# Performance work log

Hardware: AMD Instinct MI355X
Metric: run time of the kernel (lower is better)

## Reference

```python
import jax, jax.numpy as jnp
import numpy as np

MASK_OUT_VALUE = -10000.0


def setup_inputs() -> dict:
    key = jax.random.key(0)
    k1, k2, k3 = jax.random.split(key, 3)
    B, H, S, D = 2, 16, 2048, 64
    query = jax.random.normal(k1, (B, H, S, D), dtype=jnp.float32)
    key_t = jax.random.normal(k2, (B, H, S, D), dtype=jnp.float32)
    value = jax.random.normal(k3, (B, H, S, D), dtype=jnp.float32)
    # causal mask: (1, 1, S, S), True where attention is allowed
    mask = jnp.tril(jnp.ones((S, S), dtype=bool))[None, None, :, :]
    return {"query": query, "key": key_t, "value": value, "mask": mask}


def reference(query, key, value, mask):
    # scores: (B, H, S, S)
    scale = 1.0 / jnp.sqrt(jnp.asarray(query.shape[-1], query.dtype))
    attn_scores = jnp.einsum("bhqd,bhkd->bhqk", query, key) * scale
    attn_scores = jnp.where(mask, attn_scores,
                            jnp.asarray(MASK_OUT_VALUE, attn_scores.dtype))
    attn_weights = jax.nn.softmax(attn_scores, axis=-1)
    # dropout is identity (p=0 / eval mode)
    attn_output = jnp.einsum("bhqk,bhkd->bhqd", attn_weights, value)
    return attn_output
```

## Files before the change

### kernel.cpp

```cpp
#include <hip/hip_runtime.h>
#include <math.h>


#define S_LEN   2048
#define D_HEAD  64
#define SCALE_L2E 0.18033688011112042f
#define FIXM    8.0f

using bf16x8 = __attribute__((ext_vector_type(8))) short;
using f32x4  = __attribute__((ext_vector_type(4))) float;
using uint4v = __attribute__((ext_vector_type(4))) unsigned int;

__device__ __forceinline__ unsigned int rnd_bf(float f) {
  return __float_as_uint(f) + 0x8000u;
}
__device__ __forceinline__ unsigned short f2bf(float f) {
  return (unsigned short)(rnd_bf(f) >> 16);
}

__device__ __forceinline__ void gl_lds16(const unsigned short* g, unsigned short* l) {
  __builtin_amdgcn_global_load_lds(
      (const __attribute__((address_space(1))) unsigned int*)g,
      (__attribute__((address_space(3))) unsigned int*)l, 16, 0, 0);
}

__device__ __forceinline__ unsigned int cvtpk_bf16(float lo, float hi) {
  unsigned int r;
  asm("v_cvt_pk_bf16_f32 %0, %1, %2" : "=v"(r) : "v"(lo), "v"(hi));
  return r;
}
__device__ __forceinline__ void swap32(unsigned int& a, unsigned int& b) {
  asm("v_permlane32_swap_b32 %0, %1" : "+v"(a), "+v"(b));
}
__device__ __forceinline__ void swap16(unsigned int& a, unsigned int& b) {
  asm("v_permlane16_swap_b32 %0, %1" : "+v"(a), "+v"(b));
}

template <int CTRL>
__device__ __forceinline__ float dppf(float x) {
  return __builtin_bit_cast(float,
      __builtin_amdgcn_update_dpp(0, __builtin_bit_cast(int, x), CTRL, 0xF, 0xF, false));
}
__device__ __forceinline__ float rowsum16(float x) {
  x += dppf<0xB1>(x);
  x += dppf<0x4E>(x);
  x += dppf<0x124>(x);
  x += dppf<0x128>(x);
  return x;
}

__global__ __launch_bounds__(256, 4)
void prep(const float* __restrict__ Kg, const float* __restrict__ Vg,
          unsigned short* __restrict__ Kb, unsigned short* __restrict__ Vt)
{
  __shared__ __align__(16) unsigned short Lt[64][72];
  const int j = blockIdx.x, t = threadIdx.x;
  const int bh = j >> 4, seg = j & 15;
  const size_t base = (size_t)bh * (S_LEN * D_HEAD) + (size_t)seg * 128 * D_HEAD;
#pragma unroll
  for (int i = 0; i < 8; ++i) {
    const size_t idx = base + i * 1024 + t * 4;
    const f32x4 v = *(const f32x4*)(Kg + idx);
    uint2 pk;
    pk.x = (rnd_bf(v[1]) & 0xFFFF0000u) | (rnd_bf(v[0]) >> 16);
    pk.y = (rnd_bf(v[3]) & 0xFFFF0000u) | (rnd_bf(v[2]) >> 16);
    *(uint2*)(Kb + idx) = pk;
  }
  for (int h = 0; h < 2; ++h) {
    const int s0 = seg * 128 + h * 64;
    __syncthreads();
#pragma unroll
    for (int pp = 0; pp < 4; ++pp) {
      const int r = t >> 2;
      const int d0 = (t & 3) * 4 + pp * 16;
      const f32x4 v = *(const f32x4*)(Vg + (size_t)bh * (S_LEN * D_HEAD)
                                         + (size_t)(s0 + r) * D_HEAD + d0);
#pragma unroll
      for (int e = 0; e < 4; ++e) Lt[d0 + e][r] = f2bf(v[e]);
    }
    __syncthreads();
#pragma unroll
    for (int q = 0; q < 2; ++q) {
      const int d = t >> 2, ch = (t & 3) + 4 * q;
      *(uint4*)(Vt + (size_t)(bh * 64 + d) * S_LEN + s0 + ch * 8) =
          *(const uint4*)&Lt[d][ch * 8];
    }
  }
}

__global__ __launch_bounds__(256, 2)
void fa(const float* __restrict__ Qg, const unsigned short* __restrict__ Kb,
        const unsigned short* __restrict__ Vt, float* __restrict__ Og)
{
  __shared__ unsigned short Ks[2][2][64][64];
  __shared__ unsigned short Vs[2][2][64][64];

  const int id = blockIdx.x;
  const int bh = id & 31;
  const int pr = id >> 5;

  const int t    = threadIdx.x;
  const int w    = t >> 6;
  const int lane = t & 63;
  const int c    = lane & 15;
  const int quad = lane >> 4;

  const float* __restrict__ Qb = Qg + (size_t)bh * (S_LEN * D_HEAD);
  float* __restrict__ Ob = Og + (size_t)bh * (S_LEN * D_HEAD);

  const int tr0 = pr, tr1 = 31 - pr;

  int fOff[4][2];
#pragma unroll
  for (int ci = 0; ci < 4; ++ci)
#pragma unroll
    for (int h = 0; h < 2; ++h)
      fOff[ci][h] = ((ci * 16 + c) << 6) + (((h * 4 + quad) ^ (c & 7)) << 3);

  bf16x8 ones;
#pragma unroll
  for (int j = 0; j < 8; ++j) ones[j] = (short)0x3F80;

  const int rl = lane >> 3;
  const int jj = (lane & 7) ^ rl;
  auto stage1 = [&](int kt, int buf, int sub) {
#pragma unroll
    for (int n = 0; n < 2; ++n) {
      const int row = w * 16 + n * 8 + rl;
      gl_lds16(Kb + (((size_t)(bh * S_LEN + kt * 64 + row)) << 6) + jj * 8,
               &Ks[buf][sub][w * 16 + n * 8][0]);
      gl_lds16(Vt + (((size_t)(bh * 64 + row)) << 11) + kt * 64 + jj * 8,
               &Vs[buf][sub][w * 16 + n * 8][0]);
    }
  };
  auto stage_pair = [&](int it, int tr, int buf) {
    const int k0 = 2 * it;
    stage1(k0, buf, 0);
    if (k0 + 1 <= tr) stage1(k0 + 1, buf, 1);
  };

  auto smpack = [&](f32x4* sc, bf16x8& p0, bf16x8& p1) {
    unsigned int Wt[4][2];
#pragma unroll
    for (int ci = 0; ci < 4; ++ci) {
#pragma unroll
      for (int r = 0; r < 4; ++r)
        sc[ci][r] = __builtin_amdgcn_exp2f(sc[ci][r]);
      Wt[ci][0] = cvtpk_bf16(sc[ci][0], sc[ci][1]);
      Wt[ci][1] = cvtpk_bf16(sc[ci][2], sc[ci][3]);
    }
    unsigned int a00 = Wt[0][0], a02 = Wt[1][0]; swap32(a00, a02); swap16(a00, a02);
    unsigned int a01 = Wt[0][1], a03 = Wt[1][1]; swap32(a01, a03); swap16(a01, a03);
    unsigned int a10 = Wt[2][0], a12 = Wt[3][0]; swap32(a10, a12); swap16(a10, a12);
    unsigned int a11 = Wt[2][1], a13 = Wt[3][1]; swap32(a11, a13); swap16(a11, a13);
    p0 = __builtin_bit_cast(bf16x8, (uint4v){a00, a01, a02, a03});
    p1 = __builtin_bit_cast(bf16x8, (uint4v){a10, a11, a12, a13});
  };

  bf16x8 qa[2];
  f32x4 oa[4];
  f32x4 lacc;

  int buf = 0;
  stage_pair(0, tr0, 0);

#pragma unroll 1
  for (int ph = 0; ph < 2; ++ph) {
    const int tr    = ph ? tr1 : tr0;
    const int row0  = tr * 64 + w * 16;
    const int iters = (tr + 2) >> 1;

    {
      const float* qp = Qb + (size_t)(row0 + c) * D_HEAD + quad * 8;
#pragma unroll
      for (int h = 0; h < 2; ++h) {
        f32x4 a0 = *(const f32x4*)(qp + 32 * h);
        f32x4 a1 = *(const f32x4*)(qp + 32 * h + 4);
#pragma unroll
        for (int j = 0; j < 4; ++j) {
          qa[h][j]     = (short)f2bf(a0[j] * SCALE_L2E);
          qa[h][4 + j] = (short)f2bf(a1[j] * SCALE_L2E);
        }
      }
    }
#pragma unroll
    for (int i = 0; i < 4; ++i) oa[i] = (f32x4){0.f, 0.f, 0.f, 0.f};
    lacc = (f32x4){0.f, 0.f, 0.f, 0.f};

#pragma unroll 1
    for (int it = 0; it < iters; ++it) {
      __syncthreads();
      if (it + 1 < iters)  stage_pair(it + 1, tr, buf ^ 1);
      else if (ph == 0)    stage_pair(0, tr1, buf ^ 1);

      const int kt0 = 2 * it, kt1 = kt0 + 1;
      const bool has1 = (kt1 <= tr);

      const unsigned short* ks0 = &Ks[buf][0][0][0];
      const unsigned short* ks1 = &Ks[buf][1][0][0];
      bf16x8 kf0[4][2], kf1[4][2];
#pragma unroll
      for (int ci = 0; ci < 4; ++ci)
#pragma unroll
        for (int h = 0; h < 2; ++h)
          kf0[ci][h] = *(const bf16x8*)(ks0 + fOff[ci][h]);
      if (has1)
#pragma unroll
        for (int ci = 0; ci < 4; ++ci)
#pragma unroll
          for (int h = 0; h < 2; ++h)
            kf1[ci][h] = *(const bf16x8*)(ks1 + fOff[ci][h]);

      __builtin_amdgcn_s_setprio(1);
      f32x4 sc0[4], sc1[4];
#pragma unroll
      for (int ci = 0; ci < 4; ++ci) {
        f32x4 acc = (f32x4){-FIXM, -FIXM, -FIXM, -FIXM};
        acc = __builtin_amdgcn_mfma_f32_16x16x32_bf16(kf0[ci][0], qa[0], acc, 0, 0, 0);
        acc = __builtin_amdgcn_mfma_f32_16x16x32_bf16(kf0[ci][1], qa[1], acc, 0, 0, 0);
        sc0[ci] = acc;
      }
      if (has1)
#pragma unroll
        for (int ci = 0; ci < 4; ++ci) {
          f32x4 acc = (f32x4){-FIXM, -FIXM, -FIXM, -FIXM};
          acc = __builtin_amdgcn_mfma_f32_16x16x32_bf16(kf1[ci][0], qa[0], acc, 0, 0, 0);
          acc = __builtin_amdgcn_mfma_f32_16x16x32_bf16(kf1[ci][1], qa[1], acc, 0, 0, 0);
          sc1[ci] = acc;
        }

      const unsigned short* vs0 = &Vs[buf][0][0][0];
      const unsigned short* vs1 = &Vs[buf][1][0][0];
      bf16x8 vf0[4][2], vf1[4][2];
#pragma unroll
      for (int ci = 0; ci < 4; ++ci)
#pragma unroll
        for (int h = 0; h < 2; ++h)
          vf0[ci][h] = *(const bf16x8*)(vs0 + fOff[ci][h]);
      if (has1)
#pragma unroll
        for (int ci = 0; ci < 4; ++ci)
#pragma unroll
          for (int h = 0; h < 2; ++h)
            vf1[ci][h] = *(const bf16x8*)(vs1 + fOff[ci][h]);

      if (kt0 == tr) {
        const int grow = row0 + c;
#pragma unroll
        for (int ci = 0; ci < 4; ++ci)
#pragma unroll
          for (int r = 0; r < 4; ++r)
            if (kt0 * 64 + ci * 16 + quad * 4 + r > grow) sc0[ci][r] = -1e30f;
      }
      if (has1 && kt1 == tr) {
        const int grow = row0 + c;
#pragma unroll
        for (int ci = 0; ci < 4; ++ci)
#pragma unroll
          for (int r = 0; r < 4; ++r)
            if (kt1 * 64 + ci * 16 + quad * 4 + r > grow) sc1[ci][r] = -1e30f;
      }

      bf16x8 paA0, paA1, paB0, paB1;
      smpack(sc0, paA0, paA1);
      if (has1) smpack(sc1, paB0, paB1);

#pragma unroll
      for (int ci = 0; ci < 4; ++ci) {
        oa[ci] = __builtin_amdgcn_mfma_f32_16x16x32_bf16(paA0, vf0[ci][0], oa[ci], 0, 0, 0);
        oa[ci] = __builtin_amdgcn_mfma_f32_16x16x32_bf16(paA1, vf0[ci][1], oa[ci], 0, 0, 0);
      }
      lacc = __builtin_amdgcn_mfma_f32_16x16x32_bf16(paA0, ones, lacc, 0, 0, 0);
      lacc = __builtin_amdgcn_mfma_f32_16x16x32_bf16(paA1, ones, lacc, 0, 0, 0);
      if (has1) {
#pragma unroll
        for (int ci = 0; ci < 4; ++ci) {
          oa[ci] = __builtin_amdgcn_mfma_f32_16x16x32_bf16(paB0, vf1[ci][0], oa[ci], 0, 0, 0);
          oa[ci] = __builtin_amdgcn_mfma_f32_16x16x32_bf16(paB1, vf1[ci][1], oa[ci], 0, 0, 0);
        }
        lacc = __builtin_amdgcn_mfma_f32_16x16x32_bf16(paB0, ones, lacc, 0, 0, 0);
        lacc = __builtin_amdgcn_mfma_f32_16x16x32_bf16(paB1, ones, lacc, 0, 0, 0);
      }
      __builtin_amdgcn_s_setprio(0);

      buf ^= 1;
    }

    {
      float inv[4];
#pragma unroll
      for (int r = 0; r < 4; ++r) inv[r] = 1.0f / lacc[r];
#pragma unroll
      for (int ci = 0; ci < 4; ++ci)
#pragma unroll
        for (int r = 0; r < 4; ++r)
          Ob[(size_t)(row0 + quad * 4 + r) * D_HEAD + ci * 16 + c] =
              oa[ci][r] * inv[r];
    }
  }
}

__global__ __launch_bounds__(256, 4)
void fa_fb(const float* __restrict__ Qg, const float* __restrict__ Kg,
           const float* __restrict__ Vg, float* __restrict__ Og)
{
  __shared__ __align__(16) unsigned short Ksh[64][72];
  __shared__ __align__(16) unsigned short Vsh[64][72];
  __shared__ __align__(16) unsigned short Psh[4][16][72];
  const int id = blockIdx.x;
  const int bh = id & 31;
  const int p  = id >> 5;
  const int t    = threadIdx.x;
  const int w    = t >> 6;
  const int lane = t & 63;
  const int c    = lane & 15;
  const int quad = lane >> 4;
  const size_t base = (size_t)bh * (S_LEN * D_HEAD);
  const float* __restrict__ Qb = Qg + base;
  const float* __restrict__ Kb = Kg + base;
  const float* __restrict__ Vb = Vg + base;
  float* __restrict__ Ob = Og + base;
  const int wv   = w & 1;
  const int row0 = (w >= 2) ? (S_LEN - 32 * (p + 1) + 16 * wv) : (32 * p + 16 * wv);
  const int ktdiag = row0 >> 6;
  const int ktmax  = (S_LEN - 1 - 32 * p) >> 6;
  bf16x8 qa[2];
  {
    const float* qp = Qb + (size_t)(row0 + c) * D_HEAD + quad * 8;
#pragma unroll
    for (int h = 0; h < 2; ++h) {
      f32x4 a0 = *(const f32x4*)(qp + 32 * h);
      f32x4 a1 = *(const f32x4*)(qp + 32 * h + 4);
#pragma unroll
      for (int j = 0; j < 4; ++j) {
        qa[h][j]     = (short)f2bf(a0[j] * SCALE_L2E);
        qa[h][4 + j] = (short)f2bf(a1[j] * SCALE_L2E);
      }
    }
  }
  f32x4 oa[4];
  float ls[4];
#pragma unroll
  for (int i = 0; i < 4; ++i) {
    oa[i] = (f32x4){0.f, 0.f, 0.f, 0.f};
    ls[i] = 0.f;
  }
  for (int kt = 0; kt <= ktmax; ++kt) {
    __syncthreads();
    {
      const int cp = t & 15;
      const int rg = t >> 4;
      const int col0 = cp * 4;
      const int sw = (cp >> 2) << 3;
#pragma unroll
      for (int i = 0; i < 4; ++i) {
        const int row = i * 16 + rg;
        const size_t goff = (size_t)(kt * 64 + row) * D_HEAD + col0;
        const f32x4 kv = *(const f32x4*)(Kb + goff);
        const f32x4 vv = *(const f32x4*)(Vb + goff);
        const unsigned int k01 = (rnd_bf(kv[1]) & 0xFFFF0000u) | (rnd_bf(kv[0]) >> 16);
        const unsigned int k23 = (rnd_bf(kv[3]) & 0xFFFF0000u) | (rnd_bf(kv[2]) >> 16);
        *(uint2*)&Ksh[row][col0] = make_uint2(k01, k23);
        const int kz = row ^ sw;
#pragma unroll
        for (int e = 0; e < 4; ++e)
          Vsh[col0 + e][kz] = f2bf(vv[e]);
      }
    }
    __syncthreads();
    if (kt <= ktdiag) {
      bf16x8 kf[4][2], vf[4][2];
#pragma unroll
      for (int ci = 0; ci < 4; ++ci) {
        kf[ci][0] = *(const bf16x8*)&Ksh[ci * 16 + c][quad * 8];
        kf[ci][1] = *(const bf16x8*)&Ksh[ci * 16 + c][32 + quad * 8];
        vf[ci][0] = *(const bf16x8*)&Vsh[ci * 16 + c][(quad ^ ci) * 8];
        vf[ci][1] = *(const bf16x8*)&Vsh[ci * 16 + c][32 + ((quad ^ ci) * 8)];
      }
      f32x4 sc[4];
#pragma unroll
      for (int ci = 0; ci < 4; ++ci) {
        f32x4 acc = (f32x4){-FIXM, -FIXM, -FIXM, -FIXM};
        acc = __builtin_amdgcn_mfma_f32_16x16x32_bf16(qa[0], kf[ci][0], acc, 0, 0, 0);
        acc = __builtin_amdgcn_mfma_f32_16x16x32_bf16(qa[1], kf[ci][1], acc, 0, 0, 0);
        sc[ci] = acc;
      }
      if (kt == ktdiag) {
#pragma unroll
        for (int ci = 0; ci < 4; ++ci) {
          const int gcol = kt * 64 + ci * 16 + c;
#pragma unroll
          for (int r = 0; r < 4; ++r)
            if (gcol > row0 + quad * 4 + r) sc[ci][r] = -1e30f;
        }
      }
#pragma unroll
      for (int ci = 0; ci < 4; ++ci)
#pragma unroll
        for (int r = 0; r < 4; ++r)
          sc[ci][r] = __builtin_amdgcn_exp2f(sc[ci][r]);
#pragma unroll
      for (int r = 0; r < 4; ++r)
        ls[r] += (sc[0][r] + sc[1][r]) + (sc[2][r] + sc[3][r]);
#pragma unroll
      for (int ci = 0; ci < 4; ++ci)
#pragma unroll
        for (int r = 0; r < 4; ++r) {
          const int prow = quad * 4 + r;
          Psh[w][prow][(ci * 16 + c) ^ ((prow >> 3) << 3)] = f2bf(sc[ci][r]);
        }
      const int px = (c >> 3) << 3;
      const bf16x8 pa0 = *(const bf16x8*)&Psh[w][c][(quad * 8) ^ px];
      const bf16x8 pa1 = *(const bf16x8*)&Psh[w][c][((32 + quad * 8)) ^ px];
#pragma unroll
      for (int ci = 0; ci < 4; ++ci) {
        oa[ci] = __builtin_amdgcn_mfma_f32_16x16x32_bf16(pa0, vf[ci][0], oa[ci], 0, 0, 0);
        oa[ci] = __builtin_amdgcn_mfma_f32_16x16x32_bf16(pa1, vf[ci][1], oa[ci], 0, 0, 0);
      }
    }
  }
  {
    float inv[4];
#pragma unroll
    for (int r = 0; r < 4; ++r) inv[r] = 1.0f / rowsum16(ls[r]);
#pragma unroll
    for (int ci = 0; ci < 4; ++ci)
#pragma unroll
      for (int r = 0; r < 4; ++r)
        Ob[(size_t)(row0 + quad * 4 + r) * D_HEAD + ci * 16 + c] = oa[ci][r] * inv[r];
  }
}

extern "C" void kernel_launch(void* const* d_in, const int* in_sizes, int n_in,
                              void* d_out, int out_size, void* d_ws, size_t ws_size,
                              hipStream_t stream) {
  (void)in_sizes; (void)n_in; (void)out_size;
  const float* Q = (const float*)d_in[0];
  const float* K = (const float*)d_in[1];
  const float* V = (const float*)d_in[2];
  float* O = (float*)d_out;
  const size_t NEED = 2ull * 32 * S_LEN * D_HEAD * 2;
  if (ws_size >= NEED) {
    unsigned short* Kb = (unsigned short*)d_ws;
    unsigned short* Vt = Kb + (size_t)32 * S_LEN * D_HEAD;
    prep<<<dim3(512), dim3(256), 0, stream>>>(K, V, Kb, Vt);
    fa<<<dim3(512), dim3(256), 0, stream>>>(Q, Kb, Vt, O);
  } else {
    fa_fb<<<dim3(1024), dim3(256), 0, stream>>>(Q, K, V, O);
  }
}
```

Measured before the change: 130.8 us.

## Fuse K/V bf16 conversion into attention kernel, drop prep pass

```diff
diff --git a/kernel.cpp b/kernel.cpp
--- a/kernel.cpp
+++ b/kernel.cpp
@@ -18,12 +18,6 @@
   return (unsigned short)(rnd_bf(f) >> 16);
 }
 
-__device__ __forceinline__ void gl_lds16(const unsigned short* g, unsigned short* l) {
-  __builtin_amdgcn_global_load_lds(
-      (const __attribute__((address_space(1))) unsigned int*)g,
-      (__attribute__((address_space(3))) unsigned int*)l, 16, 0, 0);
-}
-
 __device__ __forceinline__ unsigned int cvtpk_bf16(float lo, float hi) {
   unsigned int r;
   asm("v_cvt_pk_bf16_f32 %0, %1, %2" : "=v"(r) : "v"(lo), "v"(hi));
@@ -36,64 +30,12 @@
   asm("v_permlane16_swap_b32 %0, %1" : "+v"(a), "+v"(b));
 }
 
-template <int CTRL>
-__device__ __forceinline__ float dppf(float x) {
-  return __builtin_bit_cast(float,
-      __builtin_amdgcn_update_dpp(0, __builtin_bit_cast(int, x), CTRL, 0xF, 0xF, false));
-}
-__device__ __forceinline__ float rowsum16(float x) {
-  x += dppf<0xB1>(x);
-  x += dppf<0x4E>(x);
-  x += dppf<0x124>(x);
-  x += dppf<0x128>(x);
-  return x;
-}
-
-__global__ __launch_bounds__(256, 4)
-void prep(const float* __restrict__ Kg, const float* __restrict__ Vg,
-          unsigned short* __restrict__ Kb, unsigned short* __restrict__ Vt)
-{
-  __shared__ __align__(16) unsigned short Lt[64][72];
-  const int j = blockIdx.x, t = threadIdx.x;
-  const int bh = j >> 4, seg = j & 15;
-  const size_t base = (size_t)bh * (S_LEN * D_HEAD) + (size_t)seg * 128 * D_HEAD;
-#pragma unroll
-  for (int i = 0; i < 8; ++i) {
-    const size_t idx = base + i * 1024 + t * 4;
-    const f32x4 v = *(const f32x4*)(Kg + idx);
-    uint2 pk;
-    pk.x = (rnd_bf(v[1]) & 0xFFFF0000u) | (rnd_bf(v[0]) >> 16);
-    pk.y = (rnd_bf(v[3]) & 0xFFFF0000u) | (rnd_bf(v[2]) >> 16);
-    *(uint2*)(Kb + idx) = pk;
-  }
-  for (int h = 0; h < 2; ++h) {
-    const int s0 = seg * 128 + h * 64;
-    __syncthreads();
-#pragma unroll
-    for (int pp = 0; pp < 4; ++pp) {
-      const int r = t >> 2;
-      const int d0 = (t & 3) * 4 + pp * 16;
-      const f32x4 v = *(const f32x4*)(Vg + (size_t)bh * (S_LEN * D_HEAD)
-                                         + (size_t)(s0 + r) * D_HEAD + d0);
-#pragma unroll
-      for (int e = 0; e < 4; ++e) Lt[d0 + e][r] = f2bf(v[e]);
-    }
-    __syncthreads();
-#pragma unroll
-    for (int q = 0; q < 2; ++q) {
-      const int d = t >> 2, ch = (t & 3) + 4 * q;
-      *(uint4*)(Vt + (size_t)(bh * 64 + d) * S_LEN + s0 + ch * 8) =
-          *(const uint4*)&Lt[d][ch * 8];
-    }
-  }
-}
-
 __global__ __launch_bounds__(256, 2)
-void fa(const float* __restrict__ Qg, const unsigned short* __restrict__ Kb,
-        const unsigned short* __restrict__ Vt, float* __restrict__ Og)
+void fa(const float* __restrict__ Qg, const float* __restrict__ Kg,
+        const float* __restrict__ Vg, float* __restrict__ Og)
 {
   __shared__ unsigned short Ks[2][2][64][64];
-  __shared__ unsigned short Vs[2][2][64][64];
+  __shared__ unsigned short Vs[2][2][64][72];
 
   const int id = blockIdx.x;
   const int bh = id & 31;
@@ -105,8 +47,11 @@
   const int c    = lane & 15;
   const int quad = lane >> 4;
 
-  const float* __restrict__ Qb = Qg + (size_t)bh * (S_LEN * D_HEAD);
-  float* __restrict__ Ob = Og + (size_t)bh * (S_LEN * D_HEAD);
+  const size_t base = (size_t)bh * (S_LEN * D_HEAD);
+  const float* __restrict__ Qb = Qg + base;
+  const float* __restrict__ Kb = Kg + base;
+  const float* __restrict__ Vb = Vg + base;
+  float* __restrict__ Ob = Og + base;
 
   const int tr0 = pr, tr1 = 31 - pr;
 
@@ -116,27 +61,62 @@
 #pragma unroll
     for (int h = 0; h < 2; ++h)
       fOff[ci][h] = ((ci * 16 + c) << 6) + (((h * 4 + quad) ^ (c & 7)) << 3);
+  int vOff[4][2];
+#pragma unroll
+  for (int ci = 0; ci < 4; ++ci)
+#pragma unroll
+    for (int h = 0; h < 2; ++h)
+      vOff[ci][h] = (ci * 16 + c) * 72 + (((h * 4 + quad) ^ ci) << 3);
 
   bf16x8 ones;
 #pragma unroll
   for (int j = 0; j < 8; ++j) ones[j] = (short)0x3F80;
 
-  const int rl = lane >> 3;
-  const int jj = (lane & 7) ^ rl;
-  auto stage1 = [&](int kt, int buf, int sub) {
-#pragma unroll
-    for (int n = 0; n < 2; ++n) {
-      const int row = w * 16 + n * 8 + rl;
-      gl_lds16(Kb + (((size_t)(bh * S_LEN + kt * 64 + row)) << 6) + jj * 8,
-               &Ks[buf][sub][w * 16 + n * 8][0]);
-      gl_lds16(Vt + (((size_t)(bh * 64 + row)) << 11) + kt * 64 + jj * 8,
-               &Vs[buf][sub][w * 16 + n * 8][0]);
-    }
+  const int sr  = lane >> 4;
+  const int sc4 = lane & 15;
+
+  f32x4 kreg[2][4], vreg[2][4];
+  auto issue_loads = [&](int n_it, int n_tr) {
+    const int k0 = 2 * n_it;
+#pragma unroll
+    for (int sub = 0; sub < 2; ++sub)
+      if (k0 + sub <= n_tr)
+#pragma unroll
+        for (int p = 0; p < 4; ++p) {
+          const int row = (k0 + sub) * 64 + w * 16 + p * 4 + sr;
+          kreg[sub][p] = *(const f32x4*)(Kb + (size_t)row * 64 + sc4 * 4);
+          vreg[sub][p] = *(const f32x4*)(Vb + (size_t)row * 64 + sc4 * 4);
+        }
   };
-  auto stage_pair = [&](int it, int tr, int buf) {
-    const int k0 = 2 * it;
-    stage1(k0, buf, 0);
-    if (k0 + 1 <= tr) stage1(k0 + 1, buf, 1);
+  auto write_K = [&](int n_it, int n_tr, int nb) {
+    const int k0 = 2 * n_it;
+#pragma unroll
+    for (int sub = 0; sub < 2; ++sub)
+      if (k0 + sub <= n_tr)
+#pragma unroll
+        for (int p = 0; p < 4; ++p) {
+          const int rl = w * 16 + p * 4 + sr;
+          uint2 pk;
+          pk.x = cvtpk_bf16(kreg[sub][p][0], kreg[sub][p][1]);
+          pk.y = cvtpk_bf16(kreg[sub][p][2], kreg[sub][p][3]);
+          const int jl = (sc4 >> 1) ^ (rl & 7);
+          *(uint2*)&Ks[nb][sub][rl][jl * 8 + (sc4 & 1) * 4] = pk;
+        }
+  };
+  auto write_V = [&](int n_it, int n_tr, int nb) {
+    const int k0 = 2 * n_it;
+#pragma unroll
+    for (int sub = 0; sub < 2; ++sub)
+      if (k0 + sub <= n_tr)
+#pragma unroll
+        for (int p = 0; p < 4; ++p) {
+          const int sl = w * 16 + p * 4 + sr;
+#pragma unroll
+          for (int e = 0; e < 4; ++e) {
+            const int d = sc4 * 4 + e;
+            Vs[nb][sub][d][sl ^ ((d >> 4) << 3)] = f2bf(vreg[sub][p][e]);
+          }
+        }
   };
 
   auto smpack = [&](f32x4* sc, bf16x8& p0, bf16x8& p1) {
@@ -162,7 +142,9 @@
   f32x4 lacc;
 
   int buf = 0;
-  stage_pair(0, tr0, 0);
+  issue_loads(0, tr0);
+  write_K(0, tr0, 0);
+  write_V(0, tr0, 0);
 
 #pragma unroll 1
   for (int ph = 0; ph < 2; ++ph) {
@@ -190,8 +172,12 @@
 #pragma unroll 1
     for (int it = 0; it < iters; ++it) {
       __syncthreads();
-      if (it + 1 < iters)  stage_pair(it + 1, tr, buf ^ 1);
-      else if (ph == 0)    stage_pair(0, tr1, buf ^ 1);
+
+      int n_it = -1, n_tr = 0;
+      if (it + 1 < iters)      { n_it = it + 1; n_tr = tr;  }
+      else if (ph == 0)        { n_it = 0;      n_tr = tr1; }
+      const bool do_stage = (n_it >= 0);
+      if (do_stage) issue_loads(n_it, n_tr);
 
       const int kt0 = 2 * it, kt1 = kt0 + 1;
       const bool has1 = (kt1 <= tr);
@@ -229,6 +215,8 @@
           sc1[ci] = acc;
         }
 
+      if (do_stage) write_K(n_it, n_tr, buf ^ 1);
+
       const unsigned short* vs0 = &Vs[buf][0][0][0];
       const unsigned short* vs1 = &Vs[buf][1][0][0];
       bf16x8 vf0[4][2], vf1[4][2];
@@ -236,13 +224,13 @@
       for (int ci = 0; ci < 4; ++ci)
 #pragma unroll
         for (int h = 0; h < 2; ++h)
-          vf0[ci][h] = *(const bf16x8*)(vs0 + fOff[ci][h]);
+          vf0[ci][h] = *(const bf16x8*)(vs0 + vOff[ci][h]);
       if (has1)
 #pragma unroll
         for (int ci = 0; ci < 4; ++ci)
 #pragma unroll
           for (int h = 0; h < 2; ++h)
-            vf1[ci][h] = *(const bf16x8*)(vs1 + fOff[ci][h]);
+            vf1[ci][h] = *(const bf16x8*)(vs1 + vOff[ci][h]);
 
       if (kt0 == tr) {
         const int grow = row0 + c;
@@ -264,6 +252,8 @@
       bf16x8 paA0, paA1, paB0, paB1;
       smpack(sc0, paA0, paA1);
       if (has1) smpack(sc1, paB0, paB1);
+
+      if (do_stage) write_V(n_it, n_tr, buf ^ 1);
 
 #pragma unroll
       for (int ci = 0; ci < 4; ++ci) {
@@ -300,152 +290,13 @@
   }
 }
 
-__global__ __launch_bounds__(256, 4)
-void fa_fb(const float* __restrict__ Qg, const float* __restrict__ Kg,
-           const float* __restrict__ Vg, float* __restrict__ Og)
-{
-  __shared__ __align__(16) unsigned short Ksh[64][72];
-  __shared__ __align__(16) unsigned short Vsh[64][72];
-  __shared__ __align__(16) unsigned short Psh[4][16][72];
-  const int id = blockIdx.x;
-  const int bh = id & 31;
-  const int p  = id >> 5;
-  const int t    = threadIdx.x;
-  const int w    = t >> 6;
-  const int lane = t & 63;
-  const int c    = lane & 15;
-  const int quad = lane >> 4;
-  const size_t base = (size_t)bh * (S_LEN * D_HEAD);
-  const float* __restrict__ Qb = Qg + base;
-  const float* __restrict__ Kb = Kg + base;
-  const float* __restrict__ Vb = Vg + base;
-  float* __restrict__ Ob = Og + base;
-  const int wv   = w & 1;
-  const int row0 = (w >= 2) ? (S_LEN - 32 * (p + 1) + 16 * wv) : (32 * p + 16 * wv);
-  const int ktdiag = row0 >> 6;
-  const int ktmax  = (S_LEN - 1 - 32 * p) >> 6;
-  bf16x8 qa[2];
-  {
-    const float* qp = Qb + (size_t)(row0 + c) * D_HEAD + quad * 8;
-#pragma unroll
-    for (int h = 0; h < 2; ++h) {
-      f32x4 a0 = *(const f32x4*)(qp + 32 * h);
-      f32x4 a1 = *(const f32x4*)(qp + 32 * h + 4);
-#pragma unroll
-      for (int j = 0; j < 4; ++j) {
-        qa[h][j]     = (short)f2bf(a0[j] * SCALE_L2E);
-        qa[h][4 + j] = (short)f2bf(a1[j] * SCALE_L2E);
-      }
-    }
-  }
-  f32x4 oa[4];
-  float ls[4];
-#pragma unroll
-  for (int i = 0; i < 4; ++i) {
-    oa[i] = (f32x4){0.f, 0.f, 0.f, 0.f};
-    ls[i] = 0.f;
-  }
-  for (int kt = 0; kt <= ktmax; ++kt) {
-    __syncthreads();
-    {
-      const int cp = t & 15;
-      const int rg = t >> 4;
-      const int col0 = cp * 4;
-      const int sw = (cp >> 2) << 3;
-#pragma unroll
-      for (int i = 0; i < 4; ++i) {
-        const int row = i * 16 + rg;
-        const size_t goff = (size_t)(kt * 64 + row) * D_HEAD + col0;
-        const f32x4 kv = *(const f32x4*)(Kb + goff);
-        const f32x4 vv = *(const f32x4*)(Vb + goff);
-        const unsigned int k01 = (rnd_bf(kv[1]) & 0xFFFF0000u) | (rnd_bf(kv[0]) >> 16);
-        const unsigned int k23 = (rnd_bf(kv[3]) & 0xFFFF0000u) | (rnd_bf(kv[2]) >> 16);
-        *(uint2*)&Ksh[row][col0] = make_uint2(k01, k23);
-        const int kz = row ^ sw;
-#pragma unroll
-        for (int e = 0; e < 4; ++e)
-          Vsh[col0 + e][kz] = f2bf(vv[e]);
-      }
-    }
-    __syncthreads();
-    if (kt <= ktdiag) {
-      bf16x8 kf[4][2], vf[4][2];
-#pragma unroll
-      for (int ci = 0; ci < 4; ++ci) {
-        kf[ci][0] = *(const bf16x8*)&Ksh[ci * 16 + c][quad * 8];
-        kf[ci][1] = *(const bf16x8*)&Ksh[ci * 16 + c][32 + quad * 8];
-        vf[ci][0] = *(const bf16x8*)&Vsh[ci * 16 + c][(quad ^ ci) * 8];
-        vf[ci][1] = *(const bf16x8*)&Vsh[ci * 16 + c][32 + ((quad ^ ci) * 8)];
-      }
-      f32x4 sc[4];
-#pragma unroll
-      for (int ci = 0; ci < 4; ++ci) {
-        f32x4 acc = (f32x4){-FIXM, -FIXM, -FIXM, -FIXM};
-        acc = __builtin_amdgcn_mfma_f32_16x16x32_bf16(qa[0], kf[ci][0], acc, 0, 0, 0);
-        acc = __builtin_amdgcn_mfma_f32_16x16x32_bf16(qa[1], kf[ci][1], acc, 0, 0, 0);
-        sc[ci] = acc;
-      }
-      if (kt == ktdiag) {
-#pragma unroll
-        for (int ci = 0; ci < 4; ++ci) {
-          const int gcol = kt * 64 + ci * 16 + c;
-#pragma unroll
-          for (int r = 0; r < 4; ++r)
-            if (gcol > row0 + quad * 4 + r) sc[ci][r] = -1e30f;
-        }
-      }
-#pragma unroll
-      for (int ci = 0; ci < 4; ++ci)
-#pragma unroll
-        for (int r = 0; r < 4; ++r)
-          sc[ci][r] = __builtin_amdgcn_exp2f(sc[ci][r]);
-#pragma unroll
-      for (int r = 0; r < 4; ++r)
-        ls[r] += (sc[0][r] + sc[1][r]) + (sc[2][r] + sc[3][r]);
-#pragma unroll
-      for (int ci = 0; ci < 4; ++ci)
-#pragma unroll
-        for (int r = 0; r < 4; ++r) {
-          const int prow = quad * 4 + r;
-          Psh[w][prow][(ci * 16 + c) ^ ((prow >> 3) << 3)] = f2bf(sc[ci][r]);
-        }
-      const int px = (c >> 3) << 3;
-      const bf16x8 pa0 = *(const bf16x8*)&Psh[w][c][(quad * 8) ^ px];
-      const bf16x8 pa1 = *(const bf16x8*)&Psh[w][c][((32 + quad * 8)) ^ px];
-#pragma unroll
-      for (int ci = 0; ci < 4; ++ci) {
-        oa[ci] = __builtin_amdgcn_mfma_f32_16x16x32_bf16(pa0, vf[ci][0], oa[ci], 0, 0, 0);
-        oa[ci] = __builtin_amdgcn_mfma_f32_16x16x32_bf16(pa1, vf[ci][1], oa[ci], 0, 0, 0);
-      }
-    }
-  }
-  {
-    float inv[4];
-#pragma unroll
-    for (int r = 0; r < 4; ++r) inv[r] = 1.0f / rowsum16(ls[r]);
-#pragma unroll
-    for (int ci = 0; ci < 4; ++ci)
-#pragma unroll
-      for (int r = 0; r < 4; ++r)
-        Ob[(size_t)(row0 + quad * 4 + r) * D_HEAD + ci * 16 + c] = oa[ci][r] * inv[r];
-  }
-}
-
 extern "C" void kernel_launch(void* const* d_in, const int* in_sizes, int n_in,
                               void* d_out, int out_size, void* d_ws, size_t ws_size,
                               hipStream_t stream) {
-  (void)in_sizes; (void)n_in; (void)out_size;
+  (void)in_sizes; (void)n_in; (void)out_size; (void)d_ws; (void)ws_size;
   const float* Q = (const float*)d_in[0];
   const float* K = (const float*)d_in[1];
   const float* V = (const float*)d_in[2];
   float* O = (float*)d_out;
-  const size_t NEED = 2ull * 32 * S_LEN * D_HEAD * 2;
-  if (ws_size >= NEED) {
-    unsigned short* Kb = (unsigned short*)d_ws;
-    unsigned short* Vt = Kb + (size_t)32 * S_LEN * D_HEAD;
-    prep<<<dim3(512), dim3(256), 0, stream>>>(K, V, Kb, Vt);
-    fa<<<dim3(512), dim3(256), 0, stream>>>(Q, Kb, Vt, O);
-  } else {
-    fa_fb<<<dim3(1024), dim3(256), 0, stream>>>(Q, K, V, O);
-  }
-}
+  fa<<<dim3(512), dim3(256), 0, stream>>>(Q, K, V, O);
+}
```

Result: slower. 180.4 us (+37.9%).

## Fuse K bf16 conversion into attention kernel via register-staged loads

Applied to the files above, without the earlier changes.

```diff
diff --git a/kernel.cpp b/kernel.cpp
--- a/kernel.cpp
+++ b/kernel.cpp
@@ -50,22 +50,11 @@
 }
 
 __global__ __launch_bounds__(256, 4)
-void prep(const float* __restrict__ Kg, const float* __restrict__ Vg,
-          unsigned short* __restrict__ Kb, unsigned short* __restrict__ Vt)
+void prep_v(const float* __restrict__ Vg, unsigned short* __restrict__ Vt)
 {
   __shared__ __align__(16) unsigned short Lt[64][72];
   const int j = blockIdx.x, t = threadIdx.x;
   const int bh = j >> 4, seg = j & 15;
-  const size_t base = (size_t)bh * (S_LEN * D_HEAD) + (size_t)seg * 128 * D_HEAD;
-#pragma unroll
-  for (int i = 0; i < 8; ++i) {
-    const size_t idx = base + i * 1024 + t * 4;
-    const f32x4 v = *(const f32x4*)(Kg + idx);
-    uint2 pk;
-    pk.x = (rnd_bf(v[1]) & 0xFFFF0000u) | (rnd_bf(v[0]) >> 16);
-    pk.y = (rnd_bf(v[3]) & 0xFFFF0000u) | (rnd_bf(v[2]) >> 16);
-    *(uint2*)(Kb + idx) = pk;
-  }
   for (int h = 0; h < 2; ++h) {
     const int s0 = seg * 128 + h * 64;
     __syncthreads();
@@ -89,7 +78,7 @@
 }
 
 __global__ __launch_bounds__(256, 2)
-void fa(const float* __restrict__ Qg, const unsigned short* __restrict__ Kb,
+void fa(const float* __restrict__ Qg, const float* __restrict__ Kg,
         const unsigned short* __restrict__ Vt, float* __restrict__ Og)
 {
   __shared__ unsigned short Ks[2][2][64][64];
@@ -105,8 +94,10 @@
   const int c    = lane & 15;
   const int quad = lane >> 4;
 
-  const float* __restrict__ Qb = Qg + (size_t)bh * (S_LEN * D_HEAD);
-  float* __restrict__ Ob = Og + (size_t)bh * (S_LEN * D_HEAD);
+  const size_t base = (size_t)bh * (S_LEN * D_HEAD);
+  const float* __restrict__ Qb = Qg + base;
+  const float* __restrict__ Kb = Kg + base;
+  float* __restrict__ Ob = Og + base;
 
   const int tr0 = pr, tr1 = 31 - pr;
 
@@ -122,21 +113,51 @@
   for (int j = 0; j < 8; ++j) ones[j] = (short)0x3F80;
 
   const int rl = lane >> 3;
-  const int jj = (lane & 7) ^ rl;
-  auto stage1 = [&](int kt, int buf, int sub) {
-#pragma unroll
-    for (int n = 0; n < 2; ++n) {
-      const int row = w * 16 + n * 8 + rl;
-      gl_lds16(Kb + (((size_t)(bh * S_LEN + kt * 64 + row)) << 6) + jj * 8,
-               &Ks[buf][sub][w * 16 + n * 8][0]);
-      gl_lds16(Vt + (((size_t)(bh * 64 + row)) << 11) + kt * 64 + jj * 8,
-               &Vs[buf][sub][w * 16 + n * 8][0]);
+  const int m8 = lane & 7;
+  const int jj = m8 ^ rl;
+
+  auto v_stage = [&](int it2, int trX, int nb) {
+#pragma unroll
+    for (int sub = 0; sub < 2; ++sub) {
+      const int kt = 2 * it2 + sub;
+      if (kt <= trX)
+#pragma unroll
+        for (int n = 0; n < 2; ++n) {
+          const int row = w * 16 + n * 8 + rl;
+          gl_lds16(Vt + (((size_t)(bh * 64 + row)) << 11) + kt * 64 + jj * 8,
+                   &Vs[nb][sub][w * 16 + n * 8][0]);
+        }
     }
   };
-  auto stage_pair = [&](int it, int tr, int buf) {
-    const int k0 = 2 * it;
-    stage1(k0, buf, 0);
-    if (k0 + 1 <= tr) stage1(k0 + 1, buf, 1);
+
+  f32x4 kst[2][2][2];
+  auto k_issue = [&](int it2, int trX) {
+    const int k0 = 2 * it2;
+#pragma unroll
+    for (int sub = 0; sub < 2; ++sub)
+      if (k0 + sub <= trX)
+#pragma unroll
+        for (int n = 0; n < 2; ++n) {
+          const int row = (k0 + sub) * 64 + w * 16 + n * 8 + rl;
+          const float* src = Kb + (size_t)row * 64 + jj * 8;
+          kst[sub][n][0] = *(const f32x4*)(src);
+          kst[sub][n][1] = *(const f32x4*)(src + 4);
+        }
+  };
+  auto k_write = [&](int it2, int trX, int nb) {
+    const int k0 = 2 * it2;
+#pragma unroll
+    for (int sub = 0; sub < 2; ++sub)
+      if (k0 + sub <= trX)
+#pragma unroll
+        for (int n = 0; n < 2; ++n) {
+          uint4v pk;
+          pk[0] = cvtpk_bf16(kst[sub][n][0][0], kst[sub][n][0][1]);
+          pk[1] = cvtpk_bf16(kst[sub][n][0][2], kst[sub][n][0][3]);
+          pk[2] = cvtpk_bf16(kst[sub][n][1][0], kst[sub][n][1][1]);
+          pk[3] = cvtpk_bf16(kst[sub][n][1][2], kst[sub][n][1][3]);
+          *(uint4v*)&Ks[nb][sub][w * 16 + n * 8 + rl][m8 * 8] = pk;
+        }
   };
 
   auto smpack = [&](f32x4* sc, bf16x8& p0, bf16x8& p1) {
@@ -162,7 +183,9 @@
   f32x4 lacc;
 
   int buf = 0;
-  stage_pair(0, tr0, 0);
+  v_stage(0, tr0, 0);
+  k_issue(0, tr0);
+  k_write(0, tr0, 0);
 
 #pragma unroll 1
   for (int ph = 0; ph < 2; ++ph) {
@@ -190,8 +213,15 @@
 #pragma unroll 1
     for (int it = 0; it < iters; ++it) {
       __syncthreads();
-      if (it + 1 < iters)  stage_pair(it + 1, tr, buf ^ 1);
-      else if (ph == 0)    stage_pair(0, tr1, buf ^ 1);
+
+      int n_it = -1, n_tr = 0;
+      if (it + 1 < iters)      { n_it = it + 1; n_tr = tr;  }
+      else if (ph == 0)        { n_it = 0;      n_tr = tr1; }
+      const bool do_stage = (n_it >= 0);
+      if (do_stage) {
+        v_stage(n_it, n_tr, buf ^ 1);
+        k_issue(n_it, n_tr);
+      }
 
       const int kt0 = 2 * it, kt1 = kt0 + 1;
       const bool has1 = (kt1 <= tr);
@@ -282,6 +312,8 @@
         lacc = __builtin_amdgcn_mfma_f32_16x16x32_bf16(paB1, ones, lacc, 0, 0, 0);
       }
       __builtin_amdgcn_s_setprio(0);
+
+      if (do_stage) k_write(n_it, n_tr, buf ^ 1);
 
       buf ^= 1;
     }
@@ -439,12 +471,11 @@
   const float* K = (const float*)d_in[1];
   const float* V = (const float*)d_in[2];
   float* O = (float*)d_out;
-  const size_t NEED = 2ull * 32 * S_LEN * D_HEAD * 2;
+  const size_t NEED = (size_t)32 * S_LEN * D_HEAD * 2;
   if (ws_size >= NEED) {
-    unsigned short* Kb = (unsigned short*)d_ws;
-    unsigned short* Vt = Kb + (size_t)32 * S_LEN * D_HEAD;
-    prep<<<dim3(512), dim3(256), 0, stream>>>(K, V, Kb, Vt);
-    fa<<<dim3(512), dim3(256), 0, stream>>>(Q, Kb, Vt, O);
+    unsigned short* Vt = (unsigned short*)d_ws;
+    prep_v<<<dim3(512), dim3(256), 0, stream>>>(V, Vt);
+    fa<<<dim3(512), dim3(256), 0, stream>>>(Q, K, Vt, O);
   } else {
     fa_fb<<<dim3(1024), dim3(256), 0, stream>>>(Q, K, V, O);
   }
```

Measured after the change: 131.6 us. Within noise of the previous version (+0.6%).
